# Kernel optimization log

Measured on AMD Instinct MI355X. Metric: run time of the kernel, lower is better.

## Reference

```python
import jax, jax.numpy as jnp
import numpy as np

MEM_CLIP = 3.0   # memory_cell_clip_value
STATE_CLIP = 3.0 # state_projection_clip_value

L, DIRS = 2, 2
B, T, D = 64, 128, 512
H, C = 512, 4096


def _run_direction(x, Wi, Wh, b, Wp, reverse):
    """One ElmoLstmCell (LSTM w/ projection + clipping) over time.
    x: [B,T,Din]; Wi: [4C,Din]; Wh: [4C,H]; b: [4C]; Wp: [H,C].
    Returns outputs [B,T,H], final h [B,H], final c [B,C]."""
    Bsz = x.shape[0]
    cdim = Wi.shape[0] // 4
    hdim = Wp.shape[0]
    h0 = jnp.zeros((Bsz, hdim), x.dtype)
    c0 = jnp.zeros((Bsz, cdim), x.dtype)
    xs = jnp.swapaxes(x, 0, 1)  # [T,B,Din]

    def step(carry, xt):
        h, c = carry
        gates = xt @ Wi.T + h @ Wh.T + b  # [B,4C]
        i, f, g, o = jnp.split(gates, 4, axis=-1)
        i = jax.nn.sigmoid(i)
        f = jax.nn.sigmoid(f)
        g = jnp.tanh(g)
        o = jax.nn.sigmoid(o)
        c_new = jnp.clip(i * g + f * c, -MEM_CLIP, MEM_CLIP)
        h_new = jnp.clip((o * jnp.tanh(c_new)) @ Wp.T, -STATE_CLIP, STATE_CLIP)
        return (h_new, c_new), h_new

    (hT, cT), ys = jax.lax.scan(step, (h0, c0), xs, reverse=reverse)
    return jnp.swapaxes(ys, 0, 1), hT, cT


def setup_inputs() -> dict:
    key = jax.random.key(0)
    ks = jax.random.split(key, 5)
    x = jax.random.normal(ks[0], (B, T, D), jnp.float32)
    Wi = jax.random.normal(ks[1], (L, DIRS, 4 * C, D), jnp.float32) / np.sqrt(D)
    Wh = jax.random.normal(ks[2], (L, DIRS, 4 * C, H), jnp.float32) / np.sqrt(H)
    b = jax.random.normal(ks[3], (L, DIRS, 4 * C), jnp.float32) * 0.01
    Wp = jax.random.normal(ks[4], (L, DIRS, H, C), jnp.float32) / np.sqrt(C)
    return {"x": x, "Wi": Wi, "Wh": Wh, "b": b, "Wp": Wp}


def reference(x, Wi, Wh, b, Wp):
    nlayers = Wi.shape[0]
    fwd_in, bwd_in = x, x
    seq_outs, hs, cs = [], [], []
    for l in range(nlayers):
        f_out, fh, fc = _run_direction(fwd_in, Wi[l, 0], Wh[l, 0], b[l, 0], Wp[l, 0], reverse=False)
        b_out, bh, bc = _run_direction(bwd_in, Wi[l, 1], Wh[l, 1], b[l, 1], Wp[l, 1], reverse=True)
        if l != 0:  # highway/residual between stacked layers
            f_out = f_out + fwd_in
            b_out = b_out + bwd_in
        fwd_in, bwd_in = f_out, b_out
        seq_outs.append(jnp.concatenate([f_out, b_out], axis=-1))  # [B,T,2H]
        hs.append(jnp.concatenate([fh, bh], axis=-1))               # [B,2H]
        cs.append(jnp.concatenate([fc, bc], axis=-1))               # [B,2C]
    return jnp.stack(seq_outs), jnp.stack(hs), jnp.stack(cs)
```

## Files before the change

kernel.cpp:

```cpp
#include <hip/hip_runtime.h>
#include <hip/hip_bf16.h>
#include <stdint.h>
#include <math.h>


#define BB 64
#define TT 128
#define DD 512
#define HH 512
#define CC 4096

typedef __bf16 v8bf __attribute__((ext_vector_type(8)));
typedef float  v4f  __attribute__((ext_vector_type(4)));
typedef short  v8s  __attribute__((ext_vector_type(8)));

__device__ __forceinline__ uint16_t f2bf(float f) {
    unsigned int x = __float_as_uint(f);
    unsigned int r = (x + 0x7fffu + ((x >> 16) & 1u)) >> 16;
    return (uint16_t)r;
}
__device__ __forceinline__ float sigm(float x) { return 1.0f / (1.0f + __expf(-x)); }

__global__ __launch_bounds__(256) void k_conv_wfull(
        const float* __restrict__ Wi, const float* __restrict__ Wh,
        uint16_t* __restrict__ Wf) {
    size_t i   = (size_t)blockIdx.x * blockDim.x + threadIdx.x;
    size_t idx = i * 8;
    size_t row = idx >> 10;
    int    k   = (int)(idx & 1023);
    const float* s = (k < 512) ? (Wh + row * 512 + k) : (Wi + row * 512 + (k - 512));
    float4 f0 = ((const float4*)s)[0];
    float4 f1 = ((const float4*)s)[1];
    v8s v;
    v[0]=f2bf(f0.x); v[1]=f2bf(f0.y); v[2]=f2bf(f0.z); v[3]=f2bf(f0.w);
    v[4]=f2bf(f1.x); v[5]=f2bf(f1.y); v[6]=f2bf(f1.z); v[7]=f2bf(f1.w);
    ((v8s*)Wf)[i] = v;
}

__global__ __launch_bounds__(256) void k_conv_plain(
        const float* __restrict__ src, uint16_t* __restrict__ dst, int n8) {
    int i = blockIdx.x * blockDim.x + threadIdx.x;
    if (i >= n8) return;
    const float4* s = (const float4*)(src + (size_t)i * 8);
    float4 f0 = s[0];
    float4 f1 = s[1];
    v8s v;
    v[0]=f2bf(f0.x); v[1]=f2bf(f0.y); v[2]=f2bf(f0.z); v[3]=f2bf(f0.w);
    v[4]=f2bf(f1.x); v[5]=f2bf(f1.y); v[6]=f2bf(f1.z); v[7]=f2bf(f1.w);
    ((v8s*)dst)[i] = v;
}

__global__ __launch_bounds__(256) void k_gates(
        const uint16_t* __restrict__ Wl,
        const float*    __restrict__ bl,
        const uint16_t* __restrict__ hprev,
        const uint16_t* __restrict__ xs0,
        const uint16_t* __restrict__ xs1,
        float*    __restrict__ c_state,
        uint16_t* __restrict__ act,
        float*    __restrict__ cs_out,
        int t_step, int flags) {
    const int dir  = blockIdx.y;
    const int bx   = blockIdx.x;
    const int tid  = threadIdx.x;
    const int w    = tid >> 6;
    const int lane = tid & 63;
    const int col  = lane & 15;
    const int quad = lane >> 4;
    const int tt   = dir ? (127 - t_step) : t_step;
    const bool first = (flags & 1), last = (flags & 2);

    const uint16_t* xsrc = dir ? xs1 : xs0;
    const uint16_t* hp   = hprev + (size_t)dir * BB * HH;
    const uint16_t* Wd   = Wl + (size_t)dir * 16384 * 1024;

    v4f acc[4][2] = {};
    const uint16_t* brow[2];
#pragma unroll
    for (int nt = 0; nt < 2; ++nt) {
        int j = w * 4096 + bx * 32 + nt * 16 + col;
        brow[nt] = Wd + (size_t)j * 1024;
    }

    int ks0 = first ? 16 : 0;
    for (int ks = ks0; ks < 32; ++ks) {
        int k = ks * 32 + quad * 8;
        v8bf a[4], bf[2];
        if (k < 512) {
#pragma unroll
            for (int mt = 0; mt < 4; ++mt) {
                int m = mt * 16 + col;
                a[mt] = *(const v8bf*)(hp + (size_t)m * HH + k);
            }
        } else {
#pragma unroll
            for (int mt = 0; mt < 4; ++mt) {
                int m = mt * 16 + col;
                a[mt] = *(const v8bf*)(xsrc + ((size_t)m * TT + tt) * DD + (k - 512));
            }
        }
#pragma unroll
        for (int nt = 0; nt < 2; ++nt) bf[nt] = *(const v8bf*)(brow[nt] + k);
#pragma unroll
        for (int mt = 0; mt < 4; ++mt)
#pragma unroll
            for (int nt = 0; nt < 2; ++nt)
                acc[mt][nt] = __builtin_amdgcn_mfma_f32_16x16x32_bf16(
                        a[mt], bf[nt], acc[mt][nt], 0, 0, 0);
    }

    __shared__ float gt[4][64][33];
#pragma unroll
    for (int mt = 0; mt < 4; ++mt)
#pragma unroll
        for (int nt = 0; nt < 2; ++nt)
#pragma unroll
            for (int r = 0; r < 4; ++r)
                gt[w][mt * 16 + quad * 4 + r][nt * 16 + col] = acc[mt][nt][r];
    __syncthreads();

    const float* bd = bl + (size_t)dir * 16384;
#pragma unroll
    for (int i = 0; i < 8; ++i) {
        int idx  = i * 256 + tid;
        int m    = idx >> 5;
        int cl   = idx & 31;
        int cell = bx * 32 + cl;
        float xi = gt[0][m][cl] + bd[cell];
        float xf = gt[1][m][cl] + bd[4096 + cell];
        float xg = gt[2][m][cl] + bd[8192 + cell];
        float xo = gt[3][m][cl] + bd[12288 + cell];
        float iv = sigm(xi), fv = sigm(xf), ov = sigm(xo);
        float gv = tanhf(xg);
        size_t cidx = ((size_t)dir * BB + m) * CC + cell;
        float cold = first ? 0.0f : c_state[cidx];
        float cn = fminf(fmaxf(iv * gv + fv * cold, -3.0f), 3.0f);
        c_state[cidx] = cn;
        act[cidx] = f2bf(ov * tanhf(cn));
        if (last) cs_out[(size_t)m * 8192 + dir * 4096 + cell] = cn;
    }
}

__global__ __launch_bounds__(256) void k_proj(
        const uint16_t* __restrict__ Wpl,
        const uint16_t* __restrict__ act,
        uint16_t* __restrict__ hout,
        uint16_t* __restrict__ hseq,
        float* __restrict__ seq_out,
        const float* __restrict__ resid,
        float* __restrict__ hs_out,
        int t_step, int last) {
    const int bn   = blockIdx.x;
    const int bm   = blockIdx.y;
    const int dir  = blockIdx.z;
    const int tid  = threadIdx.x;
    const int w    = tid >> 6;
    const int lane = tid & 63;
    const int col  = lane & 15;
    const int quad = lane >> 4;
    const int tt   = dir ? (127 - t_step) : t_step;

    const uint16_t* A  = act + ((size_t)dir * BB + bm * 16 + col) * CC;
    const uint16_t* Br = Wpl + ((size_t)dir * HH + bn * 16 + col) * CC;

    v4f acc = {};
#pragma unroll 8
    for (int ks = w * 32; ks < w * 32 + 32; ++ks) {
        int k = ks * 32 + quad * 8;
        v8bf a  = *(const v8bf*)(A + k);
        v8bf bb = *(const v8bf*)(Br + k);
        acc = __builtin_amdgcn_mfma_f32_16x16x32_bf16(a, bb, acc, 0, 0, 0);
    }
    __shared__ float red[4][256];
#pragma unroll
    for (int r = 0; r < 4; ++r)
        red[w][(quad * 4 + r) * 16 + col] = acc[r];
    __syncthreads();

    int e = tid;
    float s = red[0][e] + red[1][e] + red[2][e] + red[3][e];
    float h = fminf(fmaxf(s, -3.0f), 3.0f);
    int ml = e >> 4, nl = e & 15;
    int m = bm * 16 + ml, n = bn * 16 + nl;
    uint16_t hb = f2bf(h);
    hout[((size_t)dir * BB + m) * HH + n] = hb;
    if (hseq) hseq[(((size_t)dir * BB + m) * TT + tt) * HH + n] = hb;
    size_t so = ((size_t)m * TT + tt) * 1024 + (size_t)dir * 512 + n;
    float outv = h;
    if (resid) outv += resid[so];
    seq_out[so] = outv;
    if (last) hs_out[(size_t)m * 1024 + dir * 512 + n] = h;
}

extern "C" void kernel_launch(void* const* d_in, const int* in_sizes, int n_in,
                              void* d_out, int out_size, void* d_ws, size_t ws_size,
                              hipStream_t stream) {
    const float* x  = (const float*)d_in[0];
    const float* Wi = (const float*)d_in[1];
    const float* Wh = (const float*)d_in[2];
    const float* bb = (const float*)d_in[3];
    const float* Wp = (const float*)d_in[4];
    float* out = (float*)d_out;

    char* ws = (char*)d_ws;
    size_t off = 0;
    auto take = [&](size_t bytes) -> char* {
        char* p = ws + off;
        off = (off + bytes + 255) & ~(size_t)255;
        return p;
    };
    uint16_t* Wf   = (uint16_t*)take(2ull * 2 * 16384 * 1024 * 2);
    uint16_t* Wpb  = (uint16_t*)take(2ull * 2 * 512 * 4096 * 2);
    uint16_t* xb   = (uint16_t*)take((size_t)BB * TT * DD * 2);
    uint16_t* hseq = (uint16_t*)take(2ull * BB * TT * HH * 2);
    uint16_t* hb   = (uint16_t*)take(2ull * BB * HH * 2);
    uint16_t* actb = (uint16_t*)take(2ull * BB * CC * 2);
    float*    cst  = (float*)take(2ull * BB * CC * 4);

    hipLaunchKernelGGL(k_conv_wfull, dim3(32768), dim3(256), 0, stream, Wi, Wh, Wf);
    hipLaunchKernelGGL(k_conv_plain, dim3(4096), dim3(256), 0, stream, Wp, Wpb,
                       2 * 2 * 512 * 4096 / 8);
    hipLaunchKernelGGL(k_conv_plain, dim3(2048), dim3(256), 0, stream, x, xb,
                       BB * TT * DD / 8);

    const size_t SEQ = (size_t)BB * TT * 1024;
    float* hs_base = out + 2 * SEQ;
    float* cs_base = hs_base + 2ull * BB * 1024;

    for (int l = 0; l < 2; ++l) {
        const uint16_t* Wl  = Wf + (size_t)l * 2 * 16384 * 1024;
        const float*    blp = bb + (size_t)l * 2 * 16384;
        const uint16_t* Wpl = Wpb + (size_t)l * 2 * 512 * 4096;
        const uint16_t* xs0 = l ? hseq : xb;
        const uint16_t* xs1 = l ? hseq + (size_t)BB * TT * HH : xb;
        float* seq_l = out + (size_t)l * SEQ;
        float* cs_l  = cs_base + (size_t)l * BB * 8192;
        float* hs_l  = hs_base + (size_t)l * BB * 1024;
        for (int t = 0; t < TT; ++t) {
            int flags = (t == 0 ? 1 : 0) | (t == TT - 1 ? 2 : 0);
            hipLaunchKernelGGL(k_gates, dim3(128, 2), dim3(256), 0, stream,
                               Wl, blp, hb, xs0, xs1, cst, actb, cs_l, t, flags);
            hipLaunchKernelGGL(k_proj, dim3(32, 4, 2), dim3(256), 0, stream,
                               Wpl, actb, hb,
                               (l == 0) ? hseq : (uint16_t*)nullptr,
                               seq_l,
                               (l == 1) ? (const float*)out : (const float*)nullptr,
                               hs_l, t, (t == TT - 1) ? 1 : 0);
        }
    }
}
```

Measured before the change: 10.91 ms.

## Fuse per-step gate and projection launches into one persistent kernel with grid barriers

Replaces the 512 per-timestep launches of separate gate and projection kernels with a single persistent kernel of 256 blocks. The blocks synchronise through a software grid barrier built on atomics. The cell state now stays in registers across timesteps instead of a global buffer. The projection runs on only 64 blocks while the rest wait at the barrier, and correctness depends on all 256 blocks being co-resident.

Measured after the change: 21.89 ms. 101% more time.

```diff
diff --git a/kernel.cpp b/kernel.cpp
--- a/kernel.cpp
+++ b/kernel.cpp
@@ -9,10 +9,13 @@
 #define DD 512
 #define HH 512
 #define CC 4096
+#define NBLK 256
 
 typedef __bf16 v8bf __attribute__((ext_vector_type(8)));
 typedef float  v4f  __attribute__((ext_vector_type(4)));
 typedef short  v8s  __attribute__((ext_vector_type(8)));
+
+struct Bar { unsigned cnt[2]; unsigned gen; unsigned pad; };
 
 __device__ __forceinline__ uint16_t f2bf(float f) {
     unsigned int x = __float_as_uint(f);
@@ -20,6 +23,29 @@
     return (uint16_t)r;
 }
 __device__ __forceinline__ float sigm(float x) { return 1.0f / (1.0f + __expf(-x)); }
+
+__device__ __forceinline__ void gbar(Bar* b, unsigned* lg) {
+    __syncthreads();
+    if (threadIdx.x == 0) {
+        unsigned g = *lg;
+        __builtin_amdgcn_fence(__ATOMIC_RELEASE, "agent");
+        unsigned a = __hip_atomic_fetch_add(&b->cnt[g & 1], 1u,
+                        __ATOMIC_ACQ_REL, __HIP_MEMORY_SCOPE_AGENT);
+        if (a == NBLK - 1) {
+            __hip_atomic_store(&b->cnt[(g + 1) & 1], 0u,
+                               __ATOMIC_RELAXED, __HIP_MEMORY_SCOPE_AGENT);
+            __hip_atomic_store(&b->gen, g + 1,
+                               __ATOMIC_RELEASE, __HIP_MEMORY_SCOPE_AGENT);
+        } else {
+            while (__hip_atomic_load(&b->gen, __ATOMIC_RELAXED,
+                                     __HIP_MEMORY_SCOPE_AGENT) == g)
+                __builtin_amdgcn_s_sleep(2);
+        }
+        __builtin_amdgcn_fence(__ATOMIC_ACQUIRE, "agent");
+    }
+    *lg += 1;
+    __syncthreads();
+}
 
 __global__ __launch_bounds__(256) void k_conv_wfull(
         const float* __restrict__ Wi, const float* __restrict__ Wh,
@@ -50,146 +76,150 @@
     ((v8s*)dst)[i] = v;
 }
 
-__global__ __launch_bounds__(256) void k_gates(
-        const uint16_t* __restrict__ Wl,
-        const float*    __restrict__ bl,
-        const uint16_t* __restrict__ hprev,
-        const uint16_t* __restrict__ xs0,
-        const uint16_t* __restrict__ xs1,
-        float*    __restrict__ c_state,
-        uint16_t* __restrict__ act,
-        float*    __restrict__ cs_out,
-        int t_step, int flags) {
-    const int dir  = blockIdx.y;
-    const int bx   = blockIdx.x;
+__global__ __launch_bounds__(256) void k_persist(
+        const uint16_t* __restrict__ Wf,
+        const float*    __restrict__ bias,
+        const uint16_t* __restrict__ Wpb,
+        const uint16_t* __restrict__ xb,
+        uint16_t* __restrict__ hseq,
+        uint16_t* __restrict__ hb,
+        uint16_t* __restrict__ actb,
+        float* __restrict__ out,
+        Bar* __restrict__ bar) {
     const int tid  = threadIdx.x;
     const int w    = tid >> 6;
     const int lane = tid & 63;
     const int col  = lane & 15;
     const int quad = lane >> 4;
-    const int tt   = dir ? (127 - t_step) : t_step;
-    const bool first = (flags & 1), last = (flags & 2);
-
-    const uint16_t* xsrc = dir ? xs1 : xs0;
-    const uint16_t* hp   = hprev + (size_t)dir * BB * HH;
-    const uint16_t* Wd   = Wl + (size_t)dir * 16384 * 1024;
-
-    v4f acc[4][2] = {};
-    const uint16_t* brow[2];
-#pragma unroll
-    for (int nt = 0; nt < 2; ++nt) {
-        int j = w * 4096 + bx * 32 + nt * 16 + col;
-        brow[nt] = Wd + (size_t)j * 1024;
+    const int blk  = blockIdx.x;
+    const int gdir = blk >> 7;
+    const int gbx  = blk & 127;
+
+    const size_t SEQ = (size_t)BB * TT * 1024;
+    float* hs_base = out + 2 * SEQ;
+    float* cs_base = hs_base + 2ull * BB * 1024;
+
+    unsigned lg = 0;
+    float c_reg[8];
+    __shared__ float gt[4][64][33];
+
+    for (int l = 0; l < 2; ++l) {
+        const uint16_t* Wl  = Wf + ((size_t)l * 2 + gdir) * 16384 * 1024;
+        const float*    bd  = bias + ((size_t)l * 2 + gdir) * 16384;
+        const uint16_t* Wpl = Wpb + (size_t)l * 2 * 512 * 4096;
+        const uint16_t* xsrc = l ? (hseq + (size_t)gdir * BB * TT * HH) : xb;
+        float* seq_l = out + (size_t)l * SEQ;
+        float* cs_l  = cs_base + (size_t)l * BB * 8192;
+        float* hs_l  = hs_base + (size_t)l * BB * 1024;
+
+        for (int t = 0; t < TT; ++t) {
+            const bool first = (t == 0), last = (t == TT - 1);
+            const int tt = gdir ? (127 - t) : t;
+
+            {
+                const uint16_t* hp = hb + (size_t)gdir * BB * HH;
+                const uint16_t* brow0 = Wl + (size_t)(w * 4096 + gbx * 32 + col) * 1024;
+                const uint16_t* brow1 = brow0 + 16 * 1024;
+                v4f acc[4][2] = {};
+                int ks0 = first ? 16 : 0;
+                for (int ks = ks0; ks < 32; ++ks) {
+                    int k = ks * 32 + quad * 8;
+                    v8bf a[4], b0, b1;
+                    if (k < 512) {
+#pragma unroll
+                        for (int mt = 0; mt < 4; ++mt)
+                            a[mt] = *(const v8bf*)(hp + (size_t)(mt * 16 + col) * HH + k);
+                    } else {
+#pragma unroll
+                        for (int mt = 0; mt < 4; ++mt)
+                            a[mt] = *(const v8bf*)(xsrc + ((size_t)(mt * 16 + col) * TT + tt) * DD + (k - 512));
+                    }
+                    b0 = *(const v8bf*)(brow0 + k);
+                    b1 = *(const v8bf*)(brow1 + k);
+#pragma unroll
+                    for (int mt = 0; mt < 4; ++mt) {
+                        acc[mt][0] = __builtin_amdgcn_mfma_f32_16x16x32_bf16(a[mt], b0, acc[mt][0], 0, 0, 0);
+                        acc[mt][1] = __builtin_amdgcn_mfma_f32_16x16x32_bf16(a[mt], b1, acc[mt][1], 0, 0, 0);
+                    }
+                }
+#pragma unroll
+                for (int mt = 0; mt < 4; ++mt)
+#pragma unroll
+                    for (int nt = 0; nt < 2; ++nt)
+#pragma unroll
+                        for (int r = 0; r < 4; ++r)
+                            gt[w][mt * 16 + quad * 4 + r][nt * 16 + col] = acc[mt][nt][r];
+                __syncthreads();
+
+#pragma unroll
+                for (int i = 0; i < 8; ++i) {
+                    int idx  = i * 256 + tid;
+                    int m    = idx >> 5;
+                    int cl   = idx & 31;
+                    int cell = gbx * 32 + cl;
+                    float xi = gt[0][m][cl] + bd[cell];
+                    float xf = gt[1][m][cl] + bd[4096 + cell];
+                    float xg = gt[2][m][cl] + bd[8192 + cell];
+                    float xo = gt[3][m][cl] + bd[12288 + cell];
+                    float iv = sigm(xi), fv = sigm(xf), ov = sigm(xo);
+                    float gv = tanhf(xg);
+                    float cold = first ? 0.0f : c_reg[i];
+                    float cn = fminf(fmaxf(iv * gv + fv * cold, -3.0f), 3.0f);
+                    c_reg[i] = cn;
+                    actb[((size_t)gdir * BB + m) * CC + cell] = f2bf(ov * tanhf(cn));
+                    if (last) cs_l[(size_t)m * 8192 + gdir * 4096 + cell] = cn;
+                }
+            }
+            gbar(bar, &lg);
+
+            if (blk < 64) {
+                const int pdir = blk >> 5;
+                const int pnt  = blk & 31;
+                const int ptt  = pdir ? (127 - t) : t;
+                const uint16_t* Ad   = actb + (size_t)pdir * BB * CC;
+                const uint16_t* Brow = Wpl + ((size_t)pdir * HH + pnt * 16 + col) * CC;
+                v4f pacc[4] = {};
+                for (int it = 0; it < 32; ++it) {
+                    int k = w * 1024 + it * 32 + quad * 8;
+                    v8bf bfr = *(const v8bf*)(Brow + k);
+#pragma unroll
+                    for (int mt = 0; mt < 4; ++mt) {
+                        v8bf a = *(const v8bf*)(Ad + (size_t)(mt * 16 + col) * CC + k);
+                        pacc[mt] = __builtin_amdgcn_mfma_f32_16x16x32_bf16(a, bfr, pacc[mt], 0, 0, 0);
+                    }
+                }
+                float* red = (float*)gt;
+#pragma unroll
+                for (int mt = 0; mt < 4; ++mt)
+#pragma unroll
+                    for (int r = 0; r < 4; ++r)
+                        red[((w * 4 + mt) * 16 + quad * 4 + r) * 16 + col] = pacc[mt][r];
+                __syncthreads();
+#pragma unroll
+                for (int i = 0; i < 4; ++i) {
+                    int idx = i * 256 + tid;
+                    int m   = idx >> 4;
+                    int nl  = idx & 15;
+                    float s = red[((0 * 4 + (m >> 4)) * 16 + (m & 15)) * 16 + nl]
+                            + red[((1 * 4 + (m >> 4)) * 16 + (m & 15)) * 16 + nl]
+                            + red[((2 * 4 + (m >> 4)) * 16 + (m & 15)) * 16 + nl]
+                            + red[((3 * 4 + (m >> 4)) * 16 + (m & 15)) * 16 + nl];
+                    float h = fminf(fmaxf(s, -3.0f), 3.0f);
+                    int n = pnt * 16 + nl;
+                    uint16_t hbv = f2bf(h);
+                    hb[((size_t)pdir * BB + m) * HH + n] = hbv;
+                    if (l == 0)
+                        hseq[(((size_t)pdir * BB + m) * TT + ptt) * HH + n] = hbv;
+                    size_t so = ((size_t)m * TT + ptt) * 1024 + (size_t)pdir * 512 + n;
+                    float outv = h;
+                    if (l == 1) outv += out[so];
+                    seq_l[so] = outv;
+                    if (last) hs_l[(size_t)m * 1024 + pdir * 512 + n] = h;
+                }
+            }
+            gbar(bar, &lg);
+        }
     }
-
-    int ks0 = first ? 16 : 0;
-    for (int ks = ks0; ks < 32; ++ks) {
-        int k = ks * 32 + quad * 8;
-        v8bf a[4], bf[2];
-        if (k < 512) {
-#pragma unroll
-            for (int mt = 0; mt < 4; ++mt) {
-                int m = mt * 16 + col;
-                a[mt] = *(const v8bf*)(hp + (size_t)m * HH + k);
-            }
-        } else {
-#pragma unroll
-            for (int mt = 0; mt < 4; ++mt) {
-                int m = mt * 16 + col;
-                a[mt] = *(const v8bf*)(xsrc + ((size_t)m * TT + tt) * DD + (k - 512));
-            }
-        }
-#pragma unroll
-        for (int nt = 0; nt < 2; ++nt) bf[nt] = *(const v8bf*)(brow[nt] + k);
-#pragma unroll
-        for (int mt = 0; mt < 4; ++mt)
-#pragma unroll
-            for (int nt = 0; nt < 2; ++nt)
-                acc[mt][nt] = __builtin_amdgcn_mfma_f32_16x16x32_bf16(
-                        a[mt], bf[nt], acc[mt][nt], 0, 0, 0);
-    }
-
-    __shared__ float gt[4][64][33];
-#pragma unroll
-    for (int mt = 0; mt < 4; ++mt)
-#pragma unroll
-        for (int nt = 0; nt < 2; ++nt)
-#pragma unroll
-            for (int r = 0; r < 4; ++r)
-                gt[w][mt * 16 + quad * 4 + r][nt * 16 + col] = acc[mt][nt][r];
-    __syncthreads();
-
-    const float* bd = bl + (size_t)dir * 16384;
-#pragma unroll
-    for (int i = 0; i < 8; ++i) {
-        int idx  = i * 256 + tid;
-        int m    = idx >> 5;
-        int cl   = idx & 31;
-        int cell = bx * 32 + cl;
-        float xi = gt[0][m][cl] + bd[cell];
-        float xf = gt[1][m][cl] + bd[4096 + cell];
-        float xg = gt[2][m][cl] + bd[8192 + cell];
-        float xo = gt[3][m][cl] + bd[12288 + cell];
-        float iv = sigm(xi), fv = sigm(xf), ov = sigm(xo);
-        float gv = tanhf(xg);
-        size_t cidx = ((size_t)dir * BB + m) * CC + cell;
-        float cold = first ? 0.0f : c_state[cidx];
-        float cn = fminf(fmaxf(iv * gv + fv * cold, -3.0f), 3.0f);
-        c_state[cidx] = cn;
-        act[cidx] = f2bf(ov * tanhf(cn));
-        if (last) cs_out[(size_t)m * 8192 + dir * 4096 + cell] = cn;
-    }
-}
-
-__global__ __launch_bounds__(256) void k_proj(
-        const uint16_t* __restrict__ Wpl,
-        const uint16_t* __restrict__ act,
-        uint16_t* __restrict__ hout,
-        uint16_t* __restrict__ hseq,
-        float* __restrict__ seq_out,
-        const float* __restrict__ resid,
-        float* __restrict__ hs_out,
-        int t_step, int last) {
-    const int bn   = blockIdx.x;
-    const int bm   = blockIdx.y;
-    const int dir  = blockIdx.z;
-    const int tid  = threadIdx.x;
-    const int w    = tid >> 6;
-    const int lane = tid & 63;
-    const int col  = lane & 15;
-    const int quad = lane >> 4;
-    const int tt   = dir ? (127 - t_step) : t_step;
-
-    const uint16_t* A  = act + ((size_t)dir * BB + bm * 16 + col) * CC;
-    const uint16_t* Br = Wpl + ((size_t)dir * HH + bn * 16 + col) * CC;
-
-    v4f acc = {};
-#pragma unroll 8
-    for (int ks = w * 32; ks < w * 32 + 32; ++ks) {
-        int k = ks * 32 + quad * 8;
-        v8bf a  = *(const v8bf*)(A + k);
-        v8bf bb = *(const v8bf*)(Br + k);
-        acc = __builtin_amdgcn_mfma_f32_16x16x32_bf16(a, bb, acc, 0, 0, 0);
-    }
-    __shared__ float red[4][256];
-#pragma unroll
-    for (int r = 0; r < 4; ++r)
-        red[w][(quad * 4 + r) * 16 + col] = acc[r];
-    __syncthreads();
-
-    int e = tid;
-    float s = red[0][e] + red[1][e] + red[2][e] + red[3][e];
-    float h = fminf(fmaxf(s, -3.0f), 3.0f);
-    int ml = e >> 4, nl = e & 15;
-    int m = bm * 16 + ml, n = bn * 16 + nl;
-    uint16_t hb = f2bf(h);
-    hout[((size_t)dir * BB + m) * HH + n] = hb;
-    if (hseq) hseq[(((size_t)dir * BB + m) * TT + tt) * HH + n] = hb;
-    size_t so = ((size_t)m * TT + tt) * 1024 + (size_t)dir * 512 + n;
-    float outv = h;
-    if (resid) outv += resid[so];
-    seq_out[so] = outv;
-    if (last) hs_out[(size_t)m * 1024 + dir * 512 + n] = h;
 }
 
 extern "C" void kernel_launch(void* const* d_in, const int* in_sizes, int n_in,
@@ -215,37 +245,14 @@
     uint16_t* hseq = (uint16_t*)take(2ull * BB * TT * HH * 2);
     uint16_t* hb   = (uint16_t*)take(2ull * BB * HH * 2);
     uint16_t* actb = (uint16_t*)take(2ull * BB * CC * 2);
-    float*    cst  = (float*)take(2ull * BB * CC * 4);
-
+    Bar*      bar  = (Bar*)take(256);
+
+    hipMemsetAsync(bar, 0, 256, stream);
     hipLaunchKernelGGL(k_conv_wfull, dim3(32768), dim3(256), 0, stream, Wi, Wh, Wf);
     hipLaunchKernelGGL(k_conv_plain, dim3(4096), dim3(256), 0, stream, Wp, Wpb,
                        2 * 2 * 512 * 4096 / 8);
     hipLaunchKernelGGL(k_conv_plain, dim3(2048), dim3(256), 0, stream, x, xb,
                        BB * TT * DD / 8);
-
-    const size_t SEQ = (size_t)BB * TT * 1024;
-    float* hs_base = out + 2 * SEQ;
-    float* cs_base = hs_base + 2ull * BB * 1024;
-
-    for (int l = 0; l < 2; ++l) {
-        const uint16_t* Wl  = Wf + (size_t)l * 2 * 16384 * 1024;
-        const float*    blp = bb + (size_t)l * 2 * 16384;
-        const uint16_t* Wpl = Wpb + (size_t)l * 2 * 512 * 4096;
-        const uint16_t* xs0 = l ? hseq : xb;
-        const uint16_t* xs1 = l ? hseq + (size_t)BB * TT * HH : xb;
-        float* seq_l = out + (size_t)l * SEQ;
-        float* cs_l  = cs_base + (size_t)l * BB * 8192;
-        float* hs_l  = hs_base + (size_t)l * BB * 1024;
-        for (int t = 0; t < TT; ++t) {
-            int flags = (t == 0 ? 1 : 0) | (t == TT - 1 ? 2 : 0);
-            hipLaunchKernelGGL(k_gates, dim3(128, 2), dim3(256), 0, stream,
-                               Wl, blp, hb, xs0, xs1, cst, actb, cs_l, t, flags);
-            hipLaunchKernelGGL(k_proj, dim3(32, 4, 2), dim3(256), 0, stream,
-                               Wpl, actb, hb,
-                               (l == 0) ? hseq : (uint16_t*)nullptr,
-                               seq_l,
-                               (l == 1) ? (const float*)out : (const float*)nullptr,
-                               hs_l, t, (t == TT - 1) ? 1 : 0);
-        }
-    }
-}
+    hipLaunchKernelGGL(k_persist, dim3(NBLK), dim3(256), 0, stream,
+                       Wf, bb, Wpb, xb, hseq, hb, actb, out, bar);
+}
```
